# Kernel optimization log

Measured on AMD Instinct MI355X. Metric: run time of the kernel, lower is better.

## Reference

```python
import jax, jax.numpy as jnp
import numpy as np

B, CIN, COUT, H, W = 8, 64, 64, 56, 56
HEAD, KATT, KCONV = 1, 5, 3
HEAD_DIM = COUT // HEAD
PAD = (1 * (KATT - 1) + 1) // 2  # dilation=1 -> 2


def setup_inputs() -> dict:
    key = jax.random.key(0)
    ks = jax.random.split(key, 12)
    n = jax.random.normal
    return {
        'x': n(ks[0], (B, CIN, H, W), jnp.float32),
        'w1': n(ks[1], (COUT, CIN), jnp.float32) * 0.05,
        'b1': n(ks[2], (COUT,), jnp.float32) * 0.05,
        'w2': n(ks[3], (COUT, CIN), jnp.float32) * 0.05,
        'b2': n(ks[4], (COUT,), jnp.float32) * 0.05,
        'w3': n(ks[5], (COUT, CIN), jnp.float32) * 0.05,
        'b3': n(ks[6], (COUT,), jnp.float32) * 0.05,
        'wp': n(ks[7], (HEAD_DIM, 2), jnp.float32) * 0.05,
        'bp': n(ks[8], (HEAD_DIM,), jnp.float32) * 0.05,
        'w_fc': n(ks[9], (KCONV * KCONV, 3 * HEAD), jnp.float32) * 0.05,
        'w_dep': n(ks[10], (COUT, KCONV * KCONV, KCONV, KCONV), jnp.float32) * 0.05,
        'b_dep': n(ks[11], (COUT,), jnp.float32) * 0.05,
        'rate1': jnp.full((1,), 0.5, jnp.float32),
        'rate2': jnp.full((1,), 0.5, jnp.float32),
    }


def _conv1x1(x, w, b):
    return jnp.einsum('oc,bchw->bohw', w, x) + b[None, :, None, None]


def _unfold(x, h, w):
    # reflection-pad then extract KATTxKATT patches -> (n, c, KATT*KATT, h, w)
    p = jnp.pad(x, ((0, 0), (0, 0), (PAD, PAD), (PAD, PAD)), mode='reflect')
    return jnp.stack([p[:, :, i:i + h, j:j + w]
                      for i in range(KATT) for j in range(KATT)], axis=2)


def reference(x, w1, b1, w2, b2, w3, b3, wp, bp, w_fc, w_dep, b_dep, rate1, rate2):
    b, _, h, w = x.shape
    q = _conv1x1(x, w1, b1)
    k = _conv1x1(x, w2, b2)
    v = _conv1x1(x, w3, b3)
    head_dim = wp.shape[0]
    head = q.shape[1] // head_dim
    scaling = float(head_dim) ** -0.5

    # relative position embedding (stride=1 so q_pe == pe)
    loc_w = jnp.tile(jnp.linspace(-1.0, 1.0, w)[None, :], (h, 1))
    loc_h = jnp.tile(jnp.linspace(-1.0, 1.0, h)[:, None], (1, w))
    pe = _conv1x1(jnp.stack([loc_w, loc_h])[None], wp, bp)  # (1, head_dim, h, w)

    q_att = q.reshape(b * head, head_dim, h, w) * scaling
    k_att = k.reshape(b * head, head_dim, h, w)
    v_att = v.reshape(b * head, head_dim, h, w)

    unfold_k = _unfold(k_att, h, w)          # (b*head, d, 25, h, w)
    unfold_rpe = _unfold(pe, h, w)           # (1, d, 25, h, w)
    att = jnp.sum(q_att[:, :, None] * (unfold_k + pe[:, :, None] - unfold_rpe), axis=1)
    att = jax.nn.softmax(att, axis=1)        # softmax over the 25 window positions
    unfold_v = _unfold(v_att, h, w)
    out_att = jnp.sum(att[:, None] * unfold_v, axis=2).reshape(b, -1, h, w)

    # parallel depthwise-conv branch
    f_cat = jnp.concatenate([q.reshape(b, head, head_dim, h * w),
                             k.reshape(b, head, head_dim, h * w),
                             v.reshape(b, head, head_dim, h * w)], axis=1)  # (b, 3h, d, hw)
    f_all = jnp.einsum('oc,bcdl->bodl', w_fc, f_cat)                        # (b, 9, d, hw)
    f_conv = jnp.transpose(f_all, (0, 2, 1, 3)).reshape(b, head_dim * KCONV * KCONV, h, w)
    out_conv = jax.lax.conv_general_dilated(
        f_conv, w_dep, window_strides=(1, 1), padding=((1, 1), (1, 1)),
        feature_group_count=head_dim,
        dimension_numbers=('NCHW', 'OIHW', 'NCHW')) + b_dep[None, :, None, None]

    return rate1[0] * out_att + rate2[0] * out_conv
```

## Files before the change

### kernel.cpp

```cpp
#include <hip/hip_runtime.h>

#define HH 56
#define WWID 56
#define HWP (HH*WWID)
#define BB 8
#define CC 64
#define NPIX (BB*HWP)

__device__ __forceinline__ float grp_sum(float x) {
  int xi;
  xi = __builtin_amdgcn_update_dpp(0, __float_as_int(x), 0xB1, 0xF, 0xF, true);
  x += __int_as_float(xi);
  xi = __builtin_amdgcn_update_dpp(0, __float_as_int(x), 0x4E, 0xF, 0xF, true);
  x += __int_as_float(xi);
  xi = __builtin_amdgcn_update_dpp(0, __float_as_int(x), 0x141, 0xF, 0xF, true);
  x += __int_as_float(xi);
  xi = __builtin_amdgcn_update_dpp(0, __float_as_int(x), 0x140, 0xF, 0xF, true);
  x += __int_as_float(xi);
  return x;
}

__device__ __forceinline__ float dot4(float4 a, float4 b) {
  float t = a.x * b.x;
  t = fmaf(a.y, b.y, t);
  t = fmaf(a.z, b.z, t);
  t = fmaf(a.w, b.w, t);
  return t;
}

__device__ __forceinline__ float fcomp(const float4 v, int i) {
  return i == 0 ? v.x : i == 1 ? v.y : i == 2 ? v.z : v.w;
}

__device__ __forceinline__ int clampi(int v, int lo, int hi) {
  return v < lo ? lo : (v > hi ? hi : v);
}

__global__ __launch_bounds__(256) void prep_kernel(
    const float* __restrict__ w1, const float* __restrict__ w2, const float* __restrict__ w3,
    const float* __restrict__ w_fc, const float* __restrict__ w_dep,
    float* __restrict__ w1P, float* __restrict__ w2P, float* __restrict__ w3P,
    float* __restrict__ tab)
{
  const int gt = blockIdx.x * 256 + threadIdx.x;
  {
    const int idx = gt;
    const int c4 = idx >> 8, r = idx & 255, o = r >> 2, e = r & 3;
    const int c = c4*4 + e;
    w1P[idx] = w1[o*64 + c];
    w2P[idx] = w2[o*64 + c];
    w3P[idx] = w3[o*64 + c];
  }
  if (gt < 27*64) {
    const int d = gt & 63, bt = gt >> 6;
    const int br = bt / 9, tap = bt - br*9;
    float s = 0.f;
    #pragma unroll
    for (int oo = 0; oo < 9; ++oo)
      s += w_dep[d*81 + oo*9 + tap] * w_fc[oo*3 + br];
    tab[gt] = s;
  }
}

__global__ __launch_bounds__(256) void qkv_kernel(
    const float* __restrict__ x,
    const float* __restrict__ b1, const float* __restrict__ b2, const float* __restrict__ b3,
    const float* __restrict__ w1P, const float* __restrict__ w2P, const float* __restrict__ w3P,
    float* __restrict__ q, float* __restrict__ k, float* __restrict__ v)
{
  __shared__ float xs[64 * 32];
  const int tid = threadIdx.x;

  int bid = (int)blockIdx.x;
  bid = (bid & 7) * 98 + (bid >> 3);

  const int pix0 = bid * 32;
  const int n    = pix0 / HWP;
  const int hw0  = pix0 - n * HWP;
  const float* xb = x + (size_t)n * CC * HWP + hw0;

  #pragma unroll
  for (int r = 0; r < 2; ++r) {
    int idx = r * 256 + tid;
    int c   = idx >> 3;
    int p4  = (idx & 7) * 4;
    *reinterpret_cast<float4*>(&xs[c*32 + p4]) =
        *reinterpret_cast<const float4*>(xb + (size_t)c * HWP + p4);
  }
  __syncthreads();

  const int o = tid & 63;
  const int g = __builtin_amdgcn_readfirstlane((int)(tid >> 6));
  const float* xg = &xs[g * 8];

  float accq[8], acck[8], accv[8];
  const float bq = b1[o], bk = b2[o], bv = b3[o];
  #pragma unroll
  for (int p = 0; p < 8; ++p) { accq[p] = bq; acck[p] = bk; accv[p] = bv; }

  float4 xbuf[2][4];
  float4 wqb[2], wkb[2], wvb[2];

  xbuf[0][0] = *reinterpret_cast<const float4*>(xg + 0*32);
  xbuf[0][1] = *reinterpret_cast<const float4*>(xg + 0*32 + 4);
  xbuf[0][2] = *reinterpret_cast<const float4*>(xg + 1*32);
  xbuf[0][3] = *reinterpret_cast<const float4*>(xg + 1*32 + 4);
  wqb[0] = *reinterpret_cast<const float4*>(w1P + o*4);
  wkb[0] = *reinterpret_cast<const float4*>(w2P + o*4);
  wvb[0] = *reinterpret_cast<const float4*>(w3P + o*4);

  #pragma unroll
  for (int ph = 0; ph < 32; ++ph) {
    const int cur  = ph & 1, nxt = cur ^ 1;
    const int c4   = ph >> 1;
    const int wsel = c4 & 1;
    if (ph < 31) {
      const int cn = (ph + 1) * 2;
      xbuf[nxt][0] = *reinterpret_cast<const float4*>(xg + (cn+0)*32);
      xbuf[nxt][1] = *reinterpret_cast<const float4*>(xg + (cn+0)*32 + 4);
      xbuf[nxt][2] = *reinterpret_cast<const float4*>(xg + (cn+1)*32);
      xbuf[nxt][3] = *reinterpret_cast<const float4*>(xg + (cn+1)*32 + 4);
    }
    if (cur == 0 && c4 < 15) {
      wqb[wsel^1] = *reinterpret_cast<const float4*>(w1P + (c4+1)*256 + o*4);
      wkb[wsel^1] = *reinterpret_cast<const float4*>(w2P + (c4+1)*256 + o*4);
      wvb[wsel^1] = *reinterpret_cast<const float4*>(w3P + (c4+1)*256 + o*4);
    }
    const float wq0 = fcomp(wqb[wsel], cur*2), wq1 = fcomp(wqb[wsel], cur*2+1);
    const float wk0 = fcomp(wkb[wsel], cur*2), wk1 = fcomp(wkb[wsel], cur*2+1);
    const float wv0 = fcomp(wvb[wsel], cur*2), wv1 = fcomp(wvb[wsel], cur*2+1);
    #pragma unroll
    for (int p = 0; p < 8; ++p) {
      const float x0 = (p < 4) ? fcomp(xbuf[cur][0], p) : fcomp(xbuf[cur][1], p-4);
      const float x1 = (p < 4) ? fcomp(xbuf[cur][2], p) : fcomp(xbuf[cur][3], p-4);
      accq[p] = fmaf(wq0, x0, accq[p]);
      acck[p] = fmaf(wk0, x0, acck[p]);
      accv[p] = fmaf(wv0, x0, accv[p]);
      accq[p] = fmaf(wq1, x1, accq[p]);
      acck[p] = fmaf(wk1, x1, acck[p]);
      accv[p] = fmaf(wv1, x1, accv[p]);
    }
  }

  const int pbase = pix0 + g * 8;
  #pragma unroll
  for (int p = 0; p < 8; ++p) {
    size_t off = (size_t)(pbase + p) * 64 + o;
    q[off] = accq[p]; k[off] = acck[p]; v[off] = accv[p];
  }
}

__global__ __launch_bounds__(256) void attn_kernel(
    const float* __restrict__ q, const float* __restrict__ k, const float* __restrict__ v,
    const float* __restrict__ wp, const float* __restrict__ tab,
    const float* __restrict__ b_dep, const float* __restrict__ rate1, const float* __restrict__ rate2,
    float* __restrict__ out)
{
  __shared__ float kt[64 * 64];
  __shared__ float vt[64 * 64];
  __shared__ float qt[36 * 64];
  __shared__ float sout[64 * 17];

  const int tid = threadIdx.x;

  const int raw = (int)blockIdx.x;
  const int n   = raw & 7;
  const int t   = raw >> 3;
  const int tr  = t / 14;
  const int tc  = t - tr * 14;
  const int t0  = tr * 4;
  const int c0  = tc * 4;

  const size_t nbase = (size_t)n * HWP * 64;

  #pragma unroll
  for (int rep = 0; rep < 4; ++rep) {
    const int idx = rep * 256 + tid;
    const int pos = idx >> 4;
    const int f   = (idx & 15) * 4;
    const int r   = pos >> 3, c = pos & 7;
    const int gr  = clampi(t0 - 2 + r, 0, HH - 1);
    const int gc  = clampi(c0 - 2 + c, 0, WWID - 1);
    const size_t src = nbase + (size_t)(gr * WWID + gc) * 64 + f;
    *reinterpret_cast<float4*>(&kt[pos * 64 + f]) = *reinterpret_cast<const float4*>(k + src);
    *reinterpret_cast<float4*>(&vt[pos * 64 + f]) = *reinterpret_cast<const float4*>(v + src);
  }
  #pragma unroll
  for (int rep = 0; rep < 3; ++rep) {
    const int idx = rep * 256 + tid;
    if (idx < 576) {
      const int pos = idx >> 4;
      const int f   = (idx & 15) * 4;
      const int r   = pos / 6, c = pos - r * 6;
      const int gr  = clampi(t0 - 1 + r, 0, HH - 1);
      const int gc  = clampi(c0 - 1 + c, 0, WWID - 1);
      *reinterpret_cast<float4*>(&qt[pos * 64 + f]) =
          *reinterpret_cast<const float4*>(q + nbase + (size_t)(gr * WWID + gc) * 64 + f);
    }
  }
  __syncthreads();

  const int group = tid >> 4;
  const int sl    = tid & 15;
  const int pr    = group >> 2;
  const int pc    = group & 3;
  const int h     = t0 + pr;
  const int w     = c0 + pc;

  const float4 q4 = *reinterpret_cast<const float4*>(&qt[((pr + 1) * 6 + (pc + 1)) * 64 + sl * 4]);

  int kr[5], kc[5], hrg[5], wrg[5];
  #pragma unroll
  for (int i = 0; i < 5; ++i) {
    int tt = h + i - 2; hrg[i] = tt < 0 ? -tt : (tt >= HH ? 2*HH - 2 - tt : tt);
    kr[i] = hrg[i] - t0 + 2;
    tt = w + i - 2;     wrg[i] = tt < 0 ? -tt : (tt >= WWID ? 2*WWID - 2 - tt : tt);
    kc[i] = wrg[i] - c0 + 2;
  }

  float4 ka[5], va[5];
  #pragma unroll
  for (int j = 0; j < 5; ++j) {
    const int p0 = (kr[0] * 8 + kc[j]) * 64 + sl * 4;
    ka[j] = *reinterpret_cast<const float4*>(&kt[p0]);
    va[j] = *reinterpret_cast<const float4*>(&vt[p0]);
  }

  const float4 wa = *reinterpret_cast<const float4*>(wp + 8 * sl);
  const float4 wb = *reinterpret_cast<const float4*>(wp + 8 * sl + 4);
  const float4 wpx4 = {wa.x, wa.z, wb.x, wb.z};
  const float4 wpy4 = {wa.y, wa.w, wb.y, wb.w};
  const float qw0 = grp_sum(dot4(q4, wpx4));
  const float qw1 = grp_sum(dot4(q4, wpy4));

  const float LOG2E = 1.44269504f;
  const float L  = 0.125f * LOG2E;
  const float C  = 2.0f / 55.0f;
  const float A0 = L * qw0 * C;
  const float A1 = L * qw1 * C;

  float s = 0.f;
  float4 oatt = {0.f, 0.f, 0.f, 0.f};
  float4 cacc = {0.f, 0.f, 0.f, 0.f};

  #pragma unroll
  for (int i = 0; i < 5; ++i) {
    float4 kn[5], vn[5];
    if (i < 4) {
      #pragma unroll
      for (int j = 0; j < 5; ++j) {
        const int p1 = (kr[i+1] * 8 + kc[j]) * 64 + sl * 4;
        kn[j] = *reinterpret_cast<const float4*>(&kt[p1]);
        vn[j] = *reinterpret_cast<const float4*>(&vt[p1]);
      }
    }

    const float rh = A1 * (float)(h - hrg[i]);
    #pragma unroll
    for (int j = 0; j < 5; ++j) {
      const float d16 = grp_sum(dot4(q4, ka[j]));
      const float att = fmaf(L, d16, fmaf(A0, (float)(w - wrg[j]), rh));
      const float p = __builtin_exp2f(att);
      s += p;
      oatt.x = fmaf(p, va[j].x, oatt.x);
      oatt.y = fmaf(p, va[j].y, oatt.y);
      oatt.z = fmaf(p, va[j].z, oatt.z);
      oatt.w = fmaf(p, va[j].w, oatt.w);
    }

    if (i >= 1 && i <= 3) {
      const int kh = i - 1;
      const int hh = h + kh - 1;
      #pragma unroll
      for (int kw = 0; kw < 3; ++kw) {
        const int wc = w + kw - 1;
        const float mk = (((unsigned)hh < HH) && ((unsigned)wc < WWID)) ? 1.f : 0.f;
        const int tap = kh*3 + kw;
        const int j = kw + 1;
        const float4 tq = *reinterpret_cast<const float4*>(tab + (0*9 + tap)*64 + sl*4);
        const float4 tk = *reinterpret_cast<const float4*>(tab + (1*9 + tap)*64 + sl*4);
        const float4 tv = *reinterpret_cast<const float4*>(tab + (2*9 + tap)*64 + sl*4);
        const float4 qn = *reinterpret_cast<const float4*>(&qt[((pr + kh) * 6 + (pc + kw)) * 64 + sl * 4]);
        float sx = tq.x*qn.x; sx = fmaf(tk.x, ka[j].x, sx); sx = fmaf(tv.x, va[j].x, sx);
        float sy = tq.y*qn.y; sy = fmaf(tk.y, ka[j].y, sy); sy = fmaf(tv.y, va[j].y, sy);
        float sz = tq.z*qn.z; sz = fmaf(tk.z, ka[j].z, sz); sz = fmaf(tv.z, va[j].z, sz);
        float sw = tq.w*qn.w; sw = fmaf(tk.w, ka[j].w, sw); sw = fmaf(tv.w, va[j].w, sw);
        cacc.x = fmaf(mk, sx, cacc.x);
        cacc.y = fmaf(mk, sy, cacc.y);
        cacc.z = fmaf(mk, sz, cacc.z);
        cacc.w = fmaf(mk, sw, cacc.w);
      }
    }

    if (i < 4) {
      #pragma unroll
      for (int j = 0; j < 5; ++j) { ka[j] = kn[j]; va[j] = vn[j]; }
    }
  }

  const float inv = 1.0f / s;
  const float4 bd = *reinterpret_cast<const float4*>(b_dep + sl * 4);
  const float r1 = rate1[0] * inv;
  const float r2 = rate2[0];

  float res[4];
  res[0] = r1 * oatt.x + r2 * (cacc.x + bd.x);
  res[1] = r1 * oatt.y + r2 * (cacc.y + bd.y);
  res[2] = r1 * oatt.z + r2 * (cacc.z + bd.z);
  res[3] = r1 * oatt.w + r2 * (cacc.w + bd.w);

  #pragma unroll
  for (int e = 0; e < 4; ++e)
    sout[(4*sl + e)*17 + group] = res[e];
  __syncthreads();

  const int cc  = tid >> 2;
  const int pr2 = tid & 3;
  float4 o4 = {sout[cc*17 + pr2*4 + 0], sout[cc*17 + pr2*4 + 1],
               sout[cc*17 + pr2*4 + 2], sout[cc*17 + pr2*4 + 3]};
  *reinterpret_cast<float4*>(out + ((size_t)(n*64 + cc))*HWP + (t0 + pr2)*WWID + c0) = o4;
}

extern "C" void kernel_launch(void* const* d_in, const int* in_sizes, int n_in,
                              void* d_out, int out_size, void* d_ws, size_t ws_size,
                              hipStream_t stream) {
  const float* x     = (const float*)d_in[0];
  const float* w1    = (const float*)d_in[1];
  const float* b1    = (const float*)d_in[2];
  const float* w2    = (const float*)d_in[3];
  const float* b2    = (const float*)d_in[4];
  const float* w3    = (const float*)d_in[5];
  const float* b3    = (const float*)d_in[6];
  const float* wp    = (const float*)d_in[7];
  const float* w_fc  = (const float*)d_in[9];
  const float* w_dep = (const float*)d_in[10];
  const float* b_dep = (const float*)d_in[11];
  const float* rate1 = (const float*)d_in[12];
  const float* rate2 = (const float*)d_in[13];
  float* out = (float*)d_out;

  float* ws = (float*)d_ws;
  float* q   = ws;
  float* k   = ws + (size_t)NPIX*64;
  float* v   = ws + (size_t)2*NPIX*64;
  float* w1P = ws + (size_t)3*NPIX*64;
  float* w2P = w1P + 4096;
  float* w3P = w2P + 4096;
  float* tab = w3P + 4096;

  prep_kernel<<<16, 256, 0, stream>>>(w1, w2, w3, w_fc, w_dep, w1P, w2P, w3P, tab);
  qkv_kernel<<<NPIX/32, 256, 0, stream>>>(x, b1, b2, b3, w1P, w2P, w3P, q, k, v);
  attn_kernel<<<NPIX/16, 256, 0, stream>>>(q, k, v, wp, tab, b_dep, rate1, rate2, out);
}
```

Measured before the change: 41.89 us.

## Store q/k/v intermediates in bf16 to halve workspace traffic

The projection kernel now rounds q, k and v to bf16 before writing them to the workspace. The attention kernel loads them as bf16 into half-size shared tiles and widens them to fp32 on use. The aim is to halve global write and read traffic for the intermediates and to shrink LDS use, which may allow more blocks per CU. The k/v register prefetch of the next row is also removed in favour of per-row loads, and bf16 rounding adds numerical error to attention and conv outputs.

Result: slower. 60.56 us (+44.6%).

```diff
diff --git a/kernel.cpp b/kernel.cpp
--- a/kernel.cpp
+++ b/kernel.cpp
@@ -6,6 +6,9 @@
 #define BB 8
 #define CC 64
 #define NPIX (BB*HWP)
+
+typedef unsigned short u16;
+typedef unsigned int u32;
 
 __device__ __forceinline__ float grp_sum(float x) {
   int xi;
@@ -34,6 +37,21 @@
 
 __device__ __forceinline__ int clampi(int v, int lo, int hi) {
   return v < lo ? lo : (v > hi ? hi : v);
+}
+
+__device__ __forceinline__ u16 f2bf(float f) {
+  u32 x = __float_as_uint(f);
+  u32 r = (x + 0x7FFFu + ((x >> 16) & 1u)) >> 16;
+  return (u16)r;
+}
+
+__device__ __forceinline__ float4 ubf4(uint2 r) {
+  float4 f;
+  f.x = __uint_as_float(r.x << 16);
+  f.y = __uint_as_float(r.x & 0xFFFF0000u);
+  f.z = __uint_as_float(r.y << 16);
+  f.w = __uint_as_float(r.y & 0xFFFF0000u);
+  return f;
 }
 
 __global__ __launch_bounds__(256) void prep_kernel(
@@ -66,7 +84,7 @@
     const float* __restrict__ x,
     const float* __restrict__ b1, const float* __restrict__ b2, const float* __restrict__ b3,
     const float* __restrict__ w1P, const float* __restrict__ w2P, const float* __restrict__ w3P,
-    float* __restrict__ q, float* __restrict__ k, float* __restrict__ v)
+    u16* __restrict__ q, u16* __restrict__ k, u16* __restrict__ v)
 {
   __shared__ float xs[64 * 32];
   const int tid = threadIdx.x;
@@ -146,19 +164,19 @@
   #pragma unroll
   for (int p = 0; p < 8; ++p) {
     size_t off = (size_t)(pbase + p) * 64 + o;
-    q[off] = accq[p]; k[off] = acck[p]; v[off] = accv[p];
+    q[off] = f2bf(accq[p]); k[off] = f2bf(acck[p]); v[off] = f2bf(accv[p]);
   }
 }
 
 __global__ __launch_bounds__(256) void attn_kernel(
-    const float* __restrict__ q, const float* __restrict__ k, const float* __restrict__ v,
+    const u16* __restrict__ q, const u16* __restrict__ k, const u16* __restrict__ v,
     const float* __restrict__ wp, const float* __restrict__ tab,
     const float* __restrict__ b_dep, const float* __restrict__ rate1, const float* __restrict__ rate2,
     float* __restrict__ out)
 {
-  __shared__ float kt[64 * 64];
-  __shared__ float vt[64 * 64];
-  __shared__ float qt[36 * 64];
+  __shared__ u16 kt[64 * 64];
+  __shared__ u16 vt[64 * 64];
+  __shared__ u16 qt[36 * 64];
   __shared__ float sout[64 * 17];
 
   const int tid = threadIdx.x;
@@ -171,31 +189,33 @@
   const int t0  = tr * 4;
   const int c0  = tc * 4;
 
-  const size_t nbase = (size_t)n * HWP * 64;
-
-  #pragma unroll
-  for (int rep = 0; rep < 4; ++rep) {
+  const size_t nb2 = (size_t)n * HWP * 64;
+
+  #pragma unroll
+  for (int rep = 0; rep < 2; ++rep) {
     const int idx = rep * 256 + tid;
-    const int pos = idx >> 4;
-    const int f   = (idx & 15) * 4;
+    const int pos = idx >> 3;
+    const int ch  = idx & 7;
     const int r   = pos >> 3, c = pos & 7;
     const int gr  = clampi(t0 - 2 + r, 0, HH - 1);
     const int gc  = clampi(c0 - 2 + c, 0, WWID - 1);
-    const size_t src = nbase + (size_t)(gr * WWID + gc) * 64 + f;
-    *reinterpret_cast<float4*>(&kt[pos * 64 + f]) = *reinterpret_cast<const float4*>(k + src);
-    *reinterpret_cast<float4*>(&vt[pos * 64 + f]) = *reinterpret_cast<const float4*>(v + src);
-  }
-  #pragma unroll
-  for (int rep = 0; rep < 3; ++rep) {
+    const size_t src = nb2 + (size_t)(gr * WWID + gc) * 64;
+    reinterpret_cast<uint4*>(kt)[pos * 8 + ch] =
+        reinterpret_cast<const uint4*>(k + src)[ch];
+    reinterpret_cast<uint4*>(vt)[pos * 8 + ch] =
+        reinterpret_cast<const uint4*>(v + src)[ch];
+  }
+  #pragma unroll
+  for (int rep = 0; rep < 2; ++rep) {
     const int idx = rep * 256 + tid;
-    if (idx < 576) {
-      const int pos = idx >> 4;
-      const int f   = (idx & 15) * 4;
+    if (idx < 288) {
+      const int pos = idx >> 3;
+      const int ch  = idx & 7;
       const int r   = pos / 6, c = pos - r * 6;
       const int gr  = clampi(t0 - 1 + r, 0, HH - 1);
       const int gc  = clampi(c0 - 1 + c, 0, WWID - 1);
-      *reinterpret_cast<float4*>(&qt[pos * 64 + f]) =
-          *reinterpret_cast<const float4*>(q + nbase + (size_t)(gr * WWID + gc) * 64 + f);
+      reinterpret_cast<uint4*>(qt)[pos * 8 + ch] =
+          reinterpret_cast<const uint4*>(q + nb2 + (size_t)(gr * WWID + gc) * 64)[ch];
     }
   }
   __syncthreads();
@@ -207,7 +227,7 @@
   const int h     = t0 + pr;
   const int w     = c0 + pc;
 
-  const float4 q4 = *reinterpret_cast<const float4*>(&qt[((pr + 1) * 6 + (pc + 1)) * 64 + sl * 4]);
+  const float4 q4 = ubf4(reinterpret_cast<const uint2*>(qt)[((pr + 1) * 6 + (pc + 1)) * 16 + sl]);
 
   int kr[5], kc[5], hrg[5], wrg[5];
   #pragma unroll
@@ -216,14 +236,6 @@
     kr[i] = hrg[i] - t0 + 2;
     tt = w + i - 2;     wrg[i] = tt < 0 ? -tt : (tt >= WWID ? 2*WWID - 2 - tt : tt);
     kc[i] = wrg[i] - c0 + 2;
-  }
-
-  float4 ka[5], va[5];
-  #pragma unroll
-  for (int j = 0; j < 5; ++j) {
-    const int p0 = (kr[0] * 8 + kc[j]) * 64 + sl * 4;
-    ka[j] = *reinterpret_cast<const float4*>(&kt[p0]);
-    va[j] = *reinterpret_cast<const float4*>(&vt[p0]);
   }
 
   const float4 wa = *reinterpret_cast<const float4*>(wp + 8 * sl);
@@ -245,27 +257,25 @@
 
   #pragma unroll
   for (int i = 0; i < 5; ++i) {
-    float4 kn[5], vn[5];
-    if (i < 4) {
-      #pragma unroll
-      for (int j = 0; j < 5; ++j) {
-        const int p1 = (kr[i+1] * 8 + kc[j]) * 64 + sl * 4;
-        kn[j] = *reinterpret_cast<const float4*>(&kt[p1]);
-        vn[j] = *reinterpret_cast<const float4*>(&vt[p1]);
-      }
+    float4 kaf[5], vaf[5];
+    #pragma unroll
+    for (int j = 0; j < 5; ++j) {
+      const int p0 = (kr[i] * 8 + kc[j]) * 16 + sl;
+      kaf[j] = ubf4(reinterpret_cast<const uint2*>(kt)[p0]);
+      vaf[j] = ubf4(reinterpret_cast<const uint2*>(vt)[p0]);
     }
 
     const float rh = A1 * (float)(h - hrg[i]);
     #pragma unroll
     for (int j = 0; j < 5; ++j) {
-      const float d16 = grp_sum(dot4(q4, ka[j]));
+      const float d16 = grp_sum(dot4(q4, kaf[j]));
       const float att = fmaf(L, d16, fmaf(A0, (float)(w - wrg[j]), rh));
       const float p = __builtin_exp2f(att);
       s += p;
-      oatt.x = fmaf(p, va[j].x, oatt.x);
-      oatt.y = fmaf(p, va[j].y, oatt.y);
-      oatt.z = fmaf(p, va[j].z, oatt.z);
-      oatt.w = fmaf(p, va[j].w, oatt.w);
+      oatt.x = fmaf(p, vaf[j].x, oatt.x);
+      oatt.y = fmaf(p, vaf[j].y, oatt.y);
+      oatt.z = fmaf(p, vaf[j].z, oatt.z);
+      oatt.w = fmaf(p, vaf[j].w, oatt.w);
     }
 
     if (i >= 1 && i <= 3) {
@@ -280,21 +290,16 @@
         const float4 tq = *reinterpret_cast<const float4*>(tab + (0*9 + tap)*64 + sl*4);
         const float4 tk = *reinterpret_cast<const float4*>(tab + (1*9 + tap)*64 + sl*4);
         const float4 tv = *reinterpret_cast<const float4*>(tab + (2*9 + tap)*64 + sl*4);
-        const float4 qn = *reinterpret_cast<const float4*>(&qt[((pr + kh) * 6 + (pc + kw)) * 64 + sl * 4]);
-        float sx = tq.x*qn.x; sx = fmaf(tk.x, ka[j].x, sx); sx = fmaf(tv.x, va[j].x, sx);
-        float sy = tq.y*qn.y; sy = fmaf(tk.y, ka[j].y, sy); sy = fmaf(tv.y, va[j].y, sy);
-        float sz = tq.z*qn.z; sz = fmaf(tk.z, ka[j].z, sz); sz = fmaf(tv.z, va[j].z, sz);
-        float sw = tq.w*qn.w; sw = fmaf(tk.w, ka[j].w, sw); sw = fmaf(tv.w, va[j].w, sw);
+        const float4 qn = ubf4(reinterpret_cast<const uint2*>(qt)[((pr + kh) * 6 + (pc + kw)) * 16 + sl]);
+        float sx = tq.x*qn.x; sx = fmaf(tk.x, kaf[j].x, sx); sx = fmaf(tv.x, vaf[j].x, sx);
+        float sy = tq.y*qn.y; sy = fmaf(tk.y, kaf[j].y, sy); sy = fmaf(tv.y, vaf[j].y, sy);
+        float sz = tq.z*qn.z; sz = fmaf(tk.z, kaf[j].z, sz); sz = fmaf(tv.z, vaf[j].z, sz);
+        float sw = tq.w*qn.w; sw = fmaf(tk.w, kaf[j].w, sw); sw = fmaf(tv.w, vaf[j].w, sw);
         cacc.x = fmaf(mk, sx, cacc.x);
         cacc.y = fmaf(mk, sy, cacc.y);
         cacc.z = fmaf(mk, sz, cacc.z);
         cacc.w = fmaf(mk, sw, cacc.w);
       }
-    }
-
-    if (i < 4) {
-      #pragma unroll
-      for (int j = 0; j < 5; ++j) { ka[j] = kn[j]; va[j] = vn[j]; }
     }
   }
 
@@ -339,16 +344,16 @@
   const float* rate2 = (const float*)d_in[13];
   float* out = (float*)d_out;
 
-  float* ws = (float*)d_ws;
-  float* q   = ws;
-  float* k   = ws + (size_t)NPIX*64;
-  float* v   = ws + (size_t)2*NPIX*64;
-  float* w1P = ws + (size_t)3*NPIX*64;
+  u16* q16 = (u16*)d_ws;
+  u16* k16 = q16 + (size_t)NPIX*64;
+  u16* v16 = k16 + (size_t)NPIX*64;
+  float* wsf = (float*)(v16 + (size_t)NPIX*64);
+  float* w1P = wsf;
   float* w2P = w1P + 4096;
   float* w3P = w2P + 4096;
   float* tab = w3P + 4096;
 
   prep_kernel<<<16, 256, 0, stream>>>(w1, w2, w3, w_fc, w_dep, w1P, w2P, w3P, tab);
-  qkv_kernel<<<NPIX/32, 256, 0, stream>>>(x, b1, b2, b3, w1P, w2P, w3P, q, k, v);
-  attn_kernel<<<NPIX/16, 256, 0, stream>>>(q, k, v, wp, tab, b_dep, rate1, rate2, out);
-}
+  qkv_kernel<<<NPIX/32, 256, 0, stream>>>(x, b1, b2, b3, w1P, w2P, w3P, q16, k16, v16);
+  attn_kernel<<<NPIX/16, 256, 0, stream>>>(q16, k16, v16, wp, tab, b_dep, rate1, rate2, out);
+}
```
